# Performance work log

Hardware: AMD Instinct MI355X
Metric: run time of the kernel (lower is better)

The kernel has to match this reference:

```python
import jax, jax.numpy as jnp
import numpy as np

S, D, A, H, C = 2048, 256, 64, 8, 64  # seq_len, node_dim, num_aux, num_heads, num_channels
QUAT = 4
N_TYPES = 3  # nodes, aux, rot


def _linear_params(key, out_dim, in_dim, use_bias=True):
    kw, kb = jax.random.split(key)
    lim = 1.0 / np.sqrt(in_dim)
    W = jax.random.uniform(kw, (out_dim, in_dim), minval=-lim, maxval=lim, dtype=jnp.float32)
    if not use_bias:
        return W, None
    b = jax.random.uniform(kb, (out_dim,), minval=-lim, maxval=lim, dtype=jnp.float32)
    return W, b


def setup_inputs() -> dict:
    key = jax.random.key(0)
    ks = jax.random.split(key, 8)
    nodes = jax.random.normal(ks[0], (S, D), dtype=jnp.float32)
    aux = jax.random.normal(ks[1], (S, A), dtype=jnp.float32)
    rot = jax.random.normal(ks[2], (S, QUAT), dtype=jnp.float32)
    W_nodes, b_nodes = _linear_params(ks[3], H * C * 2, D)
    W_aux, b_aux = _linear_params(ks[4], H * C * 2, A)
    W_rot, _ = _linear_params(ks[5], H * C * 2, QUAT, use_bias=False)
    W_val, b_val = _linear_params(ks[6], D * H * N_TYPES, D)
    return {
        "nodes": nodes, "aux": aux, "rot": rot,
        "W_nodes": W_nodes, "b_nodes": b_nodes,
        "W_aux": W_aux, "b_aux": b_aux,
        "W_rot": W_rot,
        "W_val": W_val, "b_val": b_val,
    }


def reference(nodes, aux, rot, W_nodes, b_nodes, W_aux, b_aux, W_rot, W_val, b_val):
    seq_len = nodes.shape[0]
    # values: (S, 3H, D)
    val = (nodes @ W_val.T + b_val).reshape(seq_len, N_TYPES * H, -1)
    # per-source k/q: each (S, H, C)
    nodes_k, nodes_q = jnp.split((nodes @ W_nodes.T + b_nodes).reshape(seq_len, H, -1), 2, -1)
    aux_k, aux_q = jnp.split((aux @ W_aux.T + b_aux).reshape(seq_len, H, -1), 2, -1)
    rot_k, rot_q = jnp.split((rot @ W_rot.T).reshape(seq_len, H, -1), 2, -1)
    # concat along head axis -> (S, 3H, C)
    k = jnp.concatenate([nodes_k, aux_k, rot_k], axis=-2)
    q = jnp.concatenate([nodes_q, aux_q, rot_q], axis=-2)
    # (S, S, 3H) score tensor, scaled by 1/sqrt(num_heads) as in the original
    logits = jnp.einsum('ihc,jhc->ijh', k, q) / jnp.sqrt(jnp.asarray(H, nodes.dtype))
    att = jax.nn.softmax(logits, axis=-2)  # softmax over the j (key) axis
    out = jnp.einsum('ijh,jhd->id', att, val)  # (S, D)
    return out
```

## Files before the change

### kernel.cpp

```cpp
#include <hip/hip_runtime.h>

#define S_LEN 2048
#define NHEAD 24
#define CDIM 64
#define DDIM 256

typedef _Float16 f16x8 __attribute__((ext_vector_type(8)));
typedef float f32x4 __attribute__((ext_vector_type(4)));

__device__ __forceinline__ ushort f2h(float f) {
    _Float16 h = (_Float16)f;
    return __builtin_bit_cast(ushort, h);
}
__device__ __forceinline__ uint pkh(float a, float b) {
    auto v = __builtin_amdgcn_cvt_pkrtz(a, b);
    return __builtin_bit_cast(uint, v);
}
__device__ __forceinline__ uint pk2(float a, float b) {
    return (uint)f2h(a) | ((uint)f2h(b) << 16);
}

__device__ __forceinline__ int4 cvt8(const float* __restrict__ p) {
    float4 a = *(const float4*)p;
    float4 b = *(const float4*)(p + 4);
    f16x8 h;
    h[0] = (_Float16)a.x; h[1] = (_Float16)a.y;
    h[2] = (_Float16)a.z; h[3] = (_Float16)a.w;
    h[4] = (_Float16)b.x; h[5] = (_Float16)b.y;
    h[6] = (_Float16)b.z; h[7] = (_Float16)b.w;
    return __builtin_bit_cast(int4, h);
}

__global__ __launch_bounds__(256) void prep_kernel(
    const float* __restrict__ nodes, const float* __restrict__ W_val,
    float* __restrict__ out, ushort* __restrict__ nodes16, ushort* __restrict__ Wval16)
{
    int idx = blockIdx.x * 256 + threadIdx.x;
    if (idx < 131072) {
        ((float4*)out)[idx] = float4{0.f, 0.f, 0.f, 0.f};
    } else if (idx < 196608) {
        int i = idx - 131072;
        *(int4*)&nodes16[i * 8] = cvt8(&nodes[i * 8]);
    } else {
        int i = idx - 196608;
        *(int4*)&Wval16[i * 8] = cvt8(&W_val[i * 8]);
    }
}

__global__ __launch_bounds__(256) void proj_kernel(
    const float* __restrict__ nodes, const float* __restrict__ W_nodes,
    const float* __restrict__ b_nodes,
    const float* __restrict__ aux, const float* __restrict__ W_aux,
    const float* __restrict__ b_aux,
    const float* __restrict__ rot, const float* __restrict__ W_rot,
    const ushort* __restrict__ nodes16, const ushort* __restrict__ Wval16,
    const float* __restrict__ b_val,
    ushort* __restrict__ Kbuf, ushort* __restrict__ Qbuf, ushort* __restrict__ Vt)
{
    __shared__ ushort Asub[128 * 72];
    __shared__ ushort Wsub[128 * 72];
    const int blk = blockIdx.x;
    const int tid = threadIdx.x;
    const int wave = tid >> 6, lane = tid & 63;
    const int g = lane >> 4, c = lane & 15;

    if (blk < 768) {
        const int wm = wave & 1, wn = wave >> 1;
        const int m0 = (blk / 48) * 128, n0 = (blk % 48) * 128;
        const int K = 256;

        f32x4 acc[16];
#pragma unroll
        for (int t = 0; t < 16; t++) acc[t] = f32x4{0, 0, 0, 0};

        for (int k0 = 0; k0 < K; k0 += 64) {
            __syncthreads();
#pragma unroll
            for (int q = 0; q < 4; q++) {
                int i = tid + 256 * q;
                int row = i >> 3, kc = (i & 7) * 8;
                *(int4*)&Asub[row * 72 + kc] = *(const int4*)&nodes16[(m0 + row) * K + k0 + kc];
                *(int4*)&Wsub[row * 72 + kc] = *(const int4*)&Wval16[(n0 + row) * K + k0 + kc];
            }
            __syncthreads();

            f16x8 af0[4], af1[4];
#pragma unroll
            for (int mt = 0; mt < 4; mt++) {
                const ushort* Ar = &Asub[(wm * 64 + mt * 16 + c) * 72 + g * 8];
                af0[mt] = *(const f16x8*)Ar;
                af1[mt] = *(const f16x8*)(Ar + 32);
            }
#pragma unroll
            for (int nt = 0; nt < 4; nt++) {
                const ushort* Wr = &Wsub[(wn * 64 + nt * 16 + c) * 72 + g * 8];
                f16x8 bf0 = *(const f16x8*)Wr;
                f16x8 bf1 = *(const f16x8*)(Wr + 32);
#pragma unroll
                for (int mt = 0; mt < 4; mt++) {
                    acc[mt * 4 + nt] = __builtin_amdgcn_mfma_f32_16x16x32_f16(af0[mt], bf0, acc[mt * 4 + nt], 0, 0, 0);
                    acc[mt * 4 + nt] = __builtin_amdgcn_mfma_f32_16x16x32_f16(af1[mt], bf1, acc[mt * 4 + nt], 0, 0, 0);
                }
            }
        }

#pragma unroll
        for (int nt = 0; nt < 4; nt++) {
            int n = n0 + wn * 64 + nt * 16 + c;
            float bv = b_val[n];
            int h = n >> 8, d = n & 255;
#pragma unroll
            for (int mt = 0; mt < 4; mt++) {
                int m = m0 + wm * 64 + mt * 16 + g * 4;
                f32x4 v = acc[mt * 4 + nt];
                uint2 pw;
                pw.x = pk2(v[0] + bv, v[1] + bv);
                pw.y = pk2(v[2] + bv, v[3] + bv);
                *(uint2*)&Vt[(h * DDIM + d) * S_LEN + m] = pw;
            }
        }
    } else if (blk < 1792) {
        const int sub = blk - 768;
        const float *A, *W, *b;
        int K, hbase;
        if (sub < 512) { A = nodes; W = W_nodes; b = b_nodes; K = 256; hbase = 0; }
        else           { A = aux;   W = W_aux;   b = b_aux;   K = 64;  hbase = 8; }
        const int t5 = sub & 511;
        const int m0 = (t5 >> 4) * 64, n0 = (t5 & 15) * 64;
        const int srow = tid >> 2;
        const int skk = (tid & 3) * 8;

        f32x4 acc[4] = {f32x4{0,0,0,0}, f32x4{0,0,0,0}, f32x4{0,0,0,0}, f32x4{0,0,0,0}};

        for (int k0 = 0; k0 < K; k0 += 32) {
            __syncthreads();
            *(int4*)&Asub[srow * 40 + skk] = cvt8(&A[(m0 + srow) * K + k0 + skk]);
            *(int4*)&Wsub[srow * 40 + skk] = cvt8(&W[(n0 + srow) * K + k0 + skk]);
            __syncthreads();
            f16x8 af = *(const f16x8*)&Asub[(wave * 16 + c) * 40 + g * 8];
#pragma unroll
            for (int t = 0; t < 4; t++) {
                f16x8 bf = *(const f16x8*)&Wsub[(t * 16 + c) * 40 + g * 8];
                acc[t] = __builtin_amdgcn_mfma_f32_16x16x32_f16(af, bf, acc[t], 0, 0, 0);
            }
        }

#pragma unroll
        for (int t = 0; t < 4; t++) {
            int n = n0 + t * 16 + c;
            float bv = b[n];
#pragma unroll
            for (int r = 0; r < 4; r++) {
                int m = m0 + wave * 16 + g * 4 + r;
                ushort u = f2h(acc[t][r] + bv);
                int h = hbase + (n >> 7);
                int cc = n & 127;
                if (cc < 64) Kbuf[(h * S_LEN + m) * CDIM + cc] = u;
                else         Qbuf[(h * S_LEN + m) * CDIM + cc - 64] = u;
            }
        }
    } else {
        int u = (blk - 1792) * 256 + tid;
        int i = u >> 7;
        int n8 = (u & 127) * 8;
        float4 r = *(const float4*)&rot[i * 4];
        ushort pv[8];
#pragma unroll
        for (int q = 0; q < 8; q++) {
            float4 w = *(const float4*)&W_rot[(n8 + q) * 4];
            pv[q] = f2h(r.x * w.x + r.y * w.y + r.z * w.z + r.w * w.w);
        }
        int h = 16 + (n8 >> 7), cc = n8 & 127;
        int4 pkt = *(int4*)pv;
        if (cc < 64) *(int4*)&Kbuf[(h * S_LEN + i) * CDIM + cc] = pkt;
        else         *(int4*)&Qbuf[(h * S_LEN + i) * CDIM + cc - 64] = pkt;
    }
}

__global__ __launch_bounds__(256) void flash_kernel(
    const ushort* __restrict__ Kbuf, const ushort* __restrict__ Qbuf,
    const ushort* __restrict__ Vt, float* __restrict__ out)
{
    __shared__ ushort Qlds[2][64 * 72];
    __shared__ ushort Plds[2][64 * 72];
    __shared__ float  Alds[2][64];
    __shared__ int    Need[2][4] __attribute__((aligned(16)));

    const int tid = threadIdx.x;
    const int wave = tid >> 6, lane = tid & 63;
    const int g = lane >> 4, c = lane & 15;
    const int lin = blockIdx.y * 32 + blockIdx.x;
    const int xcd = lin & 7;
    const int slot = lin >> 3;
    const int h = xcd * 3 + (slot >> 5);
    const int i0 = (slot & 31) * 64;
    const float SC = 0.51006973f;
    const float THR = 8.0f;

    const ushort* Krow = &Kbuf[(h * S_LEN + i0 + wave * 16 + c) * CDIM + g * 8];
    f16x8 ka0 = *(const f16x8*)Krow;
    f16x8 ka1 = *(const f16x8*)(Krow + 32);

    const ushort* Vbase = &Vt[(h * DDIM + wave * 64 + c) * S_LEN + g * 8];

    const int qi0 = tid, qi1 = tid + 256;
    const int qr0 = qi0 >> 3, qc0 = (qi0 & 7) * 8;
    const int qr1 = qi1 >> 3, qc1 = (qi1 & 7) * 8;

    *(int4*)&Qlds[0][qr0 * 72 + qc0] =
        *(const int4*)&Qbuf[(h * S_LEN + qr0) * CDIM + qc0];
    *(int4*)&Qlds[0][qr1 * 72 + qc1] =
        *(const int4*)&Qbuf[(h * S_LEN + qr1) * CDIM + qc1];
    __syncthreads();

    f32x4 acc[16];
#pragma unroll
    for (int t = 0; t < 16; t++) acc[t] = f32x4{0, 0, 0, 0};
    float mrow = -1e30f, lrow = 0.f;

    for (int j0 = 0; j0 < S_LEN; j0 += 64) {
        const int cur = (j0 >> 6) & 1, nxt = cur ^ 1;

        const int jn = j0 + 64;
        int4 qn0 = *(const int4*)&Qbuf[(h * S_LEN + jn + qr0) * CDIM + qc0];
        int4 qn1 = *(const int4*)&Qbuf[(h * S_LEN + jn + qr1) * CDIM + qc1];

        f16x8 vf0[4], vf1[4];
#pragma unroll
        for (int t = 0; t < 4; t++) {
            const ushort* Vr = Vbase + (t * 16) * S_LEN + j0;
            vf0[t] = *(const f16x8*)Vr;
            vf1[t] = *(const f16x8*)(Vr + 32);
        }

        f32x4 Sf[4];
#pragma unroll
        for (int jc = 0; jc < 4; jc++) {
            const ushort* Qr = &Qlds[cur][(jc * 16 + c) * 72 + g * 8];
            f16x8 qb0 = *(const f16x8*)Qr;
            f16x8 qb1 = *(const f16x8*)(Qr + 32);
            f32x4 s = {0, 0, 0, 0};
            s = __builtin_amdgcn_mfma_f32_16x16x32_f16(qb0, ka0, s, 0, 0, 0);
            s = __builtin_amdgcn_mfma_f32_16x16x32_f16(qb1, ka1, s, 0, 0, 0);
            Sf[jc] = s * SC;
        }

        float tm = -1e30f;
#pragma unroll
        for (int jc = 0; jc < 4; jc++)
            tm = fmaxf(tm, fmaxf(fmaxf(Sf[jc][0], Sf[jc][1]),
                                 fmaxf(Sf[jc][2], Sf[jc][3])));
        tm = fmaxf(tm, __shfl_xor(tm, 16));
        tm = fmaxf(tm, __shfl_xor(tm, 32));

        const bool need = __any(tm > mrow + THR);
        float nm, alpha;
        if (need) {
            nm = fmaxf(tm, mrow);
            alpha = exp2f(mrow - nm);
        } else {
            nm = mrow;
            alpha = 1.0f;
        }
        if (lane == 0) Need[cur][wave] = need ? 1 : 0;

        float rs = 0.f;
#pragma unroll
        for (int jc = 0; jc < 4; jc++) {
            float p0 = exp2f(Sf[jc][0] - nm);
            float p1 = exp2f(Sf[jc][1] - nm);
            float p2 = exp2f(Sf[jc][2] - nm);
            float p3 = exp2f(Sf[jc][3] - nm);
            rs += (p0 + p1) + (p2 + p3);
            uint2 w;
            w.x = pkh(p0, p1);
            w.y = pkh(p2, p3);
            *(uint2*)&Plds[cur][(wave * 16 + c) * 72 + jc * 16 + g * 4] = w;
        }
        rs += __shfl_xor(rs, 16);
        rs += __shfl_xor(rs, 32);
        lrow = lrow * alpha + rs;
        mrow = nm;
        if (g == 0) Alds[cur][wave * 16 + c] = alpha;

        *(int4*)&Qlds[nxt][qr0 * 72 + qc0] = qn0;
        *(int4*)&Qlds[nxt][qr1 * 72 + qc1] = qn1;

        __syncthreads();

        int4 nf = *(const int4*)&Need[cur][0];
        if (nf.x | nf.y | nf.z | nf.w) {
#pragma unroll
            for (int b = 0; b < 4; b++) {
                f32x4 ab = *(const f32x4*)&Alds[cur][b * 16 + g * 4];
#pragma unroll
                for (int t = 0; t < 4; t++) acc[b * 4 + t] *= ab;
            }
        }

#pragma unroll
        for (int b = 0; b < 4; b++) {
            const ushort* Pr = &Plds[cur][(b * 16 + c) * 72 + g * 8];
            f16x8 pa0 = *(const f16x8*)Pr;
            f16x8 pa1 = *(const f16x8*)(Pr + 32);
#pragma unroll
            for (int t = 0; t < 4; t++) {
                acc[b * 4 + t] = __builtin_amdgcn_mfma_f32_16x16x32_f16(pa0, vf0[t], acc[b * 4 + t], 0, 0, 0);
                acc[b * 4 + t] = __builtin_amdgcn_mfma_f32_16x16x32_f16(pa1, vf1[t], acc[b * 4 + t], 0, 0, 0);
            }
        }
    }

    __syncthreads();
    if (g == 0) Alds[0][wave * 16 + c] = 1.0f / lrow;
    __syncthreads();
#pragma unroll
    for (int b = 0; b < 4; b++) {
        f32x4 lb = *(const f32x4*)&Alds[0][b * 16 + g * 4];
#pragma unroll
        for (int t = 0; t < 4; t++)
#pragma unroll
            for (int r = 0; r < 4; r++) {
                int i = i0 + b * 16 + g * 4 + r;
                int d = wave * 64 + t * 16 + c;
                atomicAdd(&out[i * DDIM + d], acc[b * 4 + t][r] * lb[r]);
            }
    }
}

extern "C" void kernel_launch(void* const* d_in, const int* in_sizes, int n_in,
                              void* d_out, int out_size, void* d_ws, size_t ws_size,
                              hipStream_t stream) {
    const float *nodes = 0, *aux = 0, *rot = 0, *W_nodes = 0, *b_nodes = 0,
                *W_aux = 0, *b_aux = 0, *W_rot = 0, *W_val = 0, *b_val = 0;
    int i1024[2] = {-1, -1};
    int n1024 = 0;
    for (int i = 0; i < n_in; ++i) {
        const float* p = (const float*)d_in[i];
        switch (in_sizes[i]) {
            case 524288:  nodes   = p; break;
            case 131072:  aux     = p; break;
            case 8192:    rot     = p; break;
            case 262144:  W_nodes = p; break;
            case 65536:   W_aux   = p; break;
            case 4096:    W_rot   = p; break;
            case 1572864: W_val   = p; break;
            case 6144:    b_val   = p; break;
            case 1024:    if (n1024 < 2) i1024[n1024] = i; n1024++; break;
            default: break;
        }
    }
    if (n1024 == 2) {
        b_nodes = (const float*)d_in[i1024[0]];
        b_aux   = (const float*)d_in[i1024[1]];
    }
    if (!nodes || !aux || !rot || !W_nodes || !b_nodes || !W_aux || !b_aux ||
        !W_rot || !W_val || !b_val) {
        nodes   = (const float*)d_in[0];
        aux     = (const float*)d_in[1];
        rot     = (const float*)d_in[2];
        W_nodes = (const float*)d_in[3];
        b_nodes = (const float*)d_in[4];
        W_aux   = (const float*)d_in[5];
        b_aux   = (const float*)d_in[6];
        W_rot   = (const float*)d_in[7];
        W_val   = (const float*)d_in[8];
        b_val   = (const float*)d_in[9];
    }
    float* out = (float*)d_out;

    float*  Opad = (float*)d_ws;
    ushort* Kbuf = (ushort*)(Opad + S_LEN * DDIM);
    ushort* Qbuf = Kbuf + NHEAD * S_LEN * CDIM;
    ushort* Vt   = Qbuf + NHEAD * S_LEN * CDIM;
    ushort* nodes16 = Vt + NHEAD * DDIM * S_LEN;
    ushort* Wval16  = nodes16 + 524288;

    dim3 blk(256);
    prep_kernel<<<dim3(1536), blk, 0, stream>>>(nodes, W_val, out, nodes16, Wval16);
    proj_kernel<<<dim3(2816), blk, 0, stream>>>(
        nodes, W_nodes, b_nodes, aux, W_aux, b_aux, rot, W_rot,
        nodes16, Wval16, b_val, Kbuf, Qbuf, Vt);
    flash_kernel<<<dim3(32, NHEAD), blk, 0, stream>>>(Kbuf, Qbuf, Vt, out);
}
```

Before: 252.7 us.

## Software-pipeline flash loop, fold score scale into K, defer row-sum reduce

The attention loop is restructured so each iteration computes the scores and softmax for the next tile while the PV MFMAs consume the previous tile's probabilities, with one barrier per iteration, a prologue and an epilogue. The 1/sqrt scale is folded into K during projection, which removes a multiply per score. The row-sum cross-lane shuffles are deferred until after the loop. Launch bounds now request 3 blocks per CU. Together these aim to overlap exp/softmax work with matrix work and cut per-iteration overhead, at the cost of higher register pressure and possible spills under the new occupancy constraint.

```diff
diff --git a/kernel.cpp b/kernel.cpp
--- a/kernel.cpp
+++ b/kernel.cpp
@@ -30,6 +30,8 @@
     h[6] = (_Float16)b.z; h[7] = (_Float16)b.w;
     return __builtin_bit_cast(int4, h);
 }
+
+#define SCALE_K 0.51006973f
 
 __global__ __launch_bounds__(256) void prep_kernel(
     const float* __restrict__ nodes, const float* __restrict__ W_val,
@@ -149,12 +151,13 @@
         for (int t = 0; t < 4; t++) {
             int n = n0 + t * 16 + c;
             float bv = b[n];
+            int h = hbase + (n >> 7);
+            int cc = n & 127;
+            float sc = (cc < 64) ? SCALE_K : 1.0f;
 #pragma unroll
             for (int r = 0; r < 4; r++) {
                 int m = m0 + wave * 16 + g * 4 + r;
-                ushort u = f2h(acc[t][r] + bv);
-                int h = hbase + (n >> 7);
-                int cc = n & 127;
+                ushort u = f2h((acc[t][r] + bv) * sc);
                 if (cc < 64) Kbuf[(h * S_LEN + m) * CDIM + cc] = u;
                 else         Qbuf[(h * S_LEN + m) * CDIM + cc - 64] = u;
             }
@@ -163,21 +166,23 @@
         int u = (blk - 1792) * 256 + tid;
         int i = u >> 7;
         int n8 = (u & 127) * 8;
+        int cc = n8 & 127;
+        float sc = (cc < 64) ? SCALE_K : 1.0f;
         float4 r = *(const float4*)&rot[i * 4];
         ushort pv[8];
 #pragma unroll
         for (int q = 0; q < 8; q++) {
             float4 w = *(const float4*)&W_rot[(n8 + q) * 4];
-            pv[q] = f2h(r.x * w.x + r.y * w.y + r.z * w.z + r.w * w.w);
-        }
-        int h = 16 + (n8 >> 7), cc = n8 & 127;
+            pv[q] = f2h((r.x * w.x + r.y * w.y + r.z * w.z + r.w * w.w) * sc);
+        }
+        int h = 16 + (n8 >> 7);
         int4 pkt = *(int4*)pv;
         if (cc < 64) *(int4*)&Kbuf[(h * S_LEN + i) * CDIM + cc] = pkt;
         else         *(int4*)&Qbuf[(h * S_LEN + i) * CDIM + cc - 64] = pkt;
     }
 }
 
-__global__ __launch_bounds__(256) void flash_kernel(
+__global__ __launch_bounds__(256, 3) void flash_kernel(
     const ushort* __restrict__ Kbuf, const ushort* __restrict__ Qbuf,
     const ushort* __restrict__ Vt, float* __restrict__ out)
 {
@@ -194,7 +199,6 @@
     const int slot = lin >> 3;
     const int h = xcd * 3 + (slot >> 5);
     const int i0 = (slot & 31) * 64;
-    const float SC = 0.51006973f;
     const float THR = 8.0f;
 
     const ushort* Krow = &Kbuf[(h * S_LEN + i0 + wave * 16 + c) * CDIM + g * 8];
@@ -202,49 +206,43 @@
     f16x8 ka1 = *(const f16x8*)(Krow + 32);
 
     const ushort* Vbase = &Vt[(h * DDIM + wave * 64 + c) * S_LEN + g * 8];
-
-    const int qi0 = tid, qi1 = tid + 256;
-    const int qr0 = qi0 >> 3, qc0 = (qi0 & 7) * 8;
-    const int qr1 = qi1 >> 3, qc1 = (qi1 & 7) * 8;
-
-    *(int4*)&Qlds[0][qr0 * 72 + qc0] =
-        *(const int4*)&Qbuf[(h * S_LEN + qr0) * CDIM + qc0];
-    *(int4*)&Qlds[0][qr1 * 72 + qc1] =
-        *(const int4*)&Qbuf[(h * S_LEN + qr1) * CDIM + qc1];
+    const ushort* Qh = &Qbuf[h * S_LEN * CDIM];
+
+    const int qr0 = tid >> 3, qc0 = (tid & 7) * 8;
+    const int qr1 = qr0 + 32;
+
+    *(int4*)&Qlds[0][qr0 * 72 + qc0] = *(const int4*)&Qh[qr0 * CDIM + qc0];
+    *(int4*)&Qlds[0][qr1 * 72 + qc0] = *(const int4*)&Qh[qr1 * CDIM + qc0];
+    int4 qn0 = *(const int4*)&Qh[(64 + qr0) * CDIM + qc0];
+    int4 qn1 = *(const int4*)&Qh[(64 + qr1) * CDIM + qc0];
+
+    f16x8 vf0[4], vf1[4];
+#pragma unroll
+    for (int u = 0; u < 4; u++) {
+        const ushort* Vr = Vbase + (u * 16) * S_LEN;
+        vf0[u] = *(const f16x8*)Vr;
+        vf1[u] = *(const f16x8*)(Vr + 32);
+    }
+
+    f32x4 acc[16];
+#pragma unroll
+    for (int u = 0; u < 16; u++) acc[u] = f32x4{0, 0, 0, 0};
+    float mrow = -1e30f, lrow = 0.f;
+
     __syncthreads();
 
-    f32x4 acc[16];
-#pragma unroll
-    for (int t = 0; t < 16; t++) acc[t] = f32x4{0, 0, 0, 0};
-    float mrow = -1e30f, lrow = 0.f;
-
-    for (int j0 = 0; j0 < S_LEN; j0 += 64) {
-        const int cur = (j0 >> 6) & 1, nxt = cur ^ 1;
-
-        const int jn = j0 + 64;
-        int4 qn0 = *(const int4*)&Qbuf[(h * S_LEN + jn + qr0) * CDIM + qc0];
-        int4 qn1 = *(const int4*)&Qbuf[(h * S_LEN + jn + qr1) * CDIM + qc1];
-
-        f16x8 vf0[4], vf1[4];
-#pragma unroll
-        for (int t = 0; t < 4; t++) {
-            const ushort* Vr = Vbase + (t * 16) * S_LEN + j0;
-            vf0[t] = *(const f16x8*)Vr;
-            vf1[t] = *(const f16x8*)(Vr + 32);
-        }
-
+    {
         f32x4 Sf[4];
 #pragma unroll
         for (int jc = 0; jc < 4; jc++) {
-            const ushort* Qr = &Qlds[cur][(jc * 16 + c) * 72 + g * 8];
+            const ushort* Qr = &Qlds[0][(jc * 16 + c) * 72 + g * 8];
             f16x8 qb0 = *(const f16x8*)Qr;
             f16x8 qb1 = *(const f16x8*)(Qr + 32);
             f32x4 s = {0, 0, 0, 0};
             s = __builtin_amdgcn_mfma_f32_16x16x32_f16(qb0, ka0, s, 0, 0, 0);
             s = __builtin_amdgcn_mfma_f32_16x16x32_f16(qb1, ka1, s, 0, 0, 0);
-            Sf[jc] = s * SC;
-        }
-
+            Sf[jc] = s;
+        }
         float tm = -1e30f;
 #pragma unroll
         for (int jc = 0; jc < 4; jc++)
@@ -252,18 +250,11 @@
                                  fmaxf(Sf[jc][2], Sf[jc][3])));
         tm = fmaxf(tm, __shfl_xor(tm, 16));
         tm = fmaxf(tm, __shfl_xor(tm, 32));
-
         const bool need = __any(tm > mrow + THR);
         float nm, alpha;
-        if (need) {
-            nm = fmaxf(tm, mrow);
-            alpha = exp2f(mrow - nm);
-        } else {
-            nm = mrow;
-            alpha = 1.0f;
-        }
-        if (lane == 0) Need[cur][wave] = need ? 1 : 0;
-
+        if (need) { nm = fmaxf(tm, mrow); alpha = exp2f(mrow - nm); }
+        else      { nm = mrow; alpha = 1.0f; }
+        if (lane == 0) Need[0][wave] = need ? 1 : 0;
         float rs = 0.f;
 #pragma unroll
         for (int jc = 0; jc < 4; jc++) {
@@ -275,18 +266,35 @@
             uint2 w;
             w.x = pkh(p0, p1);
             w.y = pkh(p2, p3);
-            *(uint2*)&Plds[cur][(wave * 16 + c) * 72 + jc * 16 + g * 4] = w;
-        }
-        rs += __shfl_xor(rs, 16);
-        rs += __shfl_xor(rs, 32);
+            *(uint2*)&Plds[0][(wave * 16 + c) * 72 + jc * 16 + g * 4] = w;
+        }
         lrow = lrow * alpha + rs;
         mrow = nm;
-        if (g == 0) Alds[cur][wave * 16 + c] = alpha;
-
-        *(int4*)&Qlds[nxt][qr0 * 72 + qc0] = qn0;
-        *(int4*)&Qlds[nxt][qr1 * 72 + qc1] = qn1;
-
+        if (g == 0) Alds[0][wave * 16 + c] = alpha;
+    }
+    *(int4*)&Qlds[1][qr0 * 72 + qc0] = qn0;
+    *(int4*)&Qlds[1][qr1 * 72 + qc0] = qn1;
+
+    for (int t = 0; t < 31; ++t) {
+        const int cur = t & 1, nxt = cur ^ 1;
         __syncthreads();
+
+        if (t < 30) {
+            qn0 = *(const int4*)&Qh[((t + 2) * 64 + qr0) * CDIM + qc0];
+            qn1 = *(const int4*)&Qh[((t + 2) * 64 + qr1) * CDIM + qc0];
+        }
+
+        f32x4 Sf[4];
+#pragma unroll
+        for (int jc = 0; jc < 4; jc++) {
+            const ushort* Qr = &Qlds[nxt][(jc * 16 + c) * 72 + g * 8];
+            f16x8 qb0 = *(const f16x8*)Qr;
+            f16x8 qb1 = *(const f16x8*)(Qr + 32);
+            f32x4 s = {0, 0, 0, 0};
+            s = __builtin_amdgcn_mfma_f32_16x16x32_f16(qb0, ka0, s, 0, 0, 0);
+            s = __builtin_amdgcn_mfma_f32_16x16x32_f16(qb1, ka1, s, 0, 0, 0);
+            Sf[jc] = s;
+        }
 
         int4 nf = *(const int4*)&Need[cur][0];
         if (nf.x | nf.y | nf.z | nf.w) {
@@ -294,7 +302,7 @@
             for (int b = 0; b < 4; b++) {
                 f32x4 ab = *(const f32x4*)&Alds[cur][b * 16 + g * 4];
 #pragma unroll
-                for (int t = 0; t < 4; t++) acc[b * 4 + t] *= ab;
+                for (int u = 0; u < 4; u++) acc[b * 4 + u] *= ab;
             }
         }
 
@@ -304,12 +312,82 @@
             f16x8 pa0 = *(const f16x8*)Pr;
             f16x8 pa1 = *(const f16x8*)(Pr + 32);
 #pragma unroll
-            for (int t = 0; t < 4; t++) {
-                acc[b * 4 + t] = __builtin_amdgcn_mfma_f32_16x16x32_f16(pa0, vf0[t], acc[b * 4 + t], 0, 0, 0);
-                acc[b * 4 + t] = __builtin_amdgcn_mfma_f32_16x16x32_f16(pa1, vf1[t], acc[b * 4 + t], 0, 0, 0);
-            }
-        }
-    }
+            for (int u = 0; u < 4; u++) {
+                acc[b * 4 + u] = __builtin_amdgcn_mfma_f32_16x16x32_f16(pa0, vf0[u], acc[b * 4 + u], 0, 0, 0);
+                acc[b * 4 + u] = __builtin_amdgcn_mfma_f32_16x16x32_f16(pa1, vf1[u], acc[b * 4 + u], 0, 0, 0);
+            }
+        }
+
+#pragma unroll
+        for (int u = 0; u < 4; u++) {
+            const ushort* Vr = Vbase + (u * 16) * S_LEN + (t + 1) * 64;
+            vf0[u] = *(const f16x8*)Vr;
+            vf1[u] = *(const f16x8*)(Vr + 32);
+        }
+
+        {
+            float tm = -1e30f;
+#pragma unroll
+            for (int jc = 0; jc < 4; jc++)
+                tm = fmaxf(tm, fmaxf(fmaxf(Sf[jc][0], Sf[jc][1]),
+                                     fmaxf(Sf[jc][2], Sf[jc][3])));
+            tm = fmaxf(tm, __shfl_xor(tm, 16));
+            tm = fmaxf(tm, __shfl_xor(tm, 32));
+            const bool need = __any(tm > mrow + THR);
+            float nm, alpha;
+            if (need) { nm = fmaxf(tm, mrow); alpha = exp2f(mrow - nm); }
+            else      { nm = mrow; alpha = 1.0f; }
+            if (lane == 0) Need[nxt][wave] = need ? 1 : 0;
+            float rs = 0.f;
+#pragma unroll
+            for (int jc = 0; jc < 4; jc++) {
+                float p0 = exp2f(Sf[jc][0] - nm);
+                float p1 = exp2f(Sf[jc][1] - nm);
+                float p2 = exp2f(Sf[jc][2] - nm);
+                float p3 = exp2f(Sf[jc][3] - nm);
+                rs += (p0 + p1) + (p2 + p3);
+                uint2 w;
+                w.x = pkh(p0, p1);
+                w.y = pkh(p2, p3);
+                *(uint2*)&Plds[nxt][(wave * 16 + c) * 72 + jc * 16 + g * 4] = w;
+            }
+            lrow = lrow * alpha + rs;
+            mrow = nm;
+            if (g == 0) Alds[nxt][wave * 16 + c] = alpha;
+        }
+
+        if (t < 30) {
+            *(int4*)&Qlds[cur][qr0 * 72 + qc0] = qn0;
+            *(int4*)&Qlds[cur][qr1 * 72 + qc0] = qn1;
+        }
+    }
+
+    __syncthreads();
+    {
+        int4 nf = *(const int4*)&Need[1][0];
+        if (nf.x | nf.y | nf.z | nf.w) {
+#pragma unroll
+            for (int b = 0; b < 4; b++) {
+                f32x4 ab = *(const f32x4*)&Alds[1][b * 16 + g * 4];
+#pragma unroll
+                for (int u = 0; u < 4; u++) acc[b * 4 + u] *= ab;
+            }
+        }
+#pragma unroll
+        for (int b = 0; b < 4; b++) {
+            const ushort* Pr = &Plds[1][(b * 16 + c) * 72 + g * 8];
+            f16x8 pa0 = *(const f16x8*)Pr;
+            f16x8 pa1 = *(const f16x8*)(Pr + 32);
+#pragma unroll
+            for (int u = 0; u < 4; u++) {
+                acc[b * 4 + u] = __builtin_amdgcn_mfma_f32_16x16x32_f16(pa0, vf0[u], acc[b * 4 + u], 0, 0, 0);
+                acc[b * 4 + u] = __builtin_amdgcn_mfma_f32_16x16x32_f16(pa1, vf1[u], acc[b * 4 + u], 0, 0, 0);
+            }
+        }
+    }
+
+    lrow += __shfl_xor(lrow, 16);
+    lrow += __shfl_xor(lrow, 32);
 
     __syncthreads();
     if (g == 0) Alds[0][wave * 16 + c] = 1.0f / lrow;
@@ -318,12 +396,12 @@
     for (int b = 0; b < 4; b++) {
         f32x4 lb = *(const f32x4*)&Alds[0][b * 16 + g * 4];
 #pragma unroll
-        for (int t = 0; t < 4; t++)
+        for (int u = 0; u < 4; u++)
 #pragma unroll
             for (int r = 0; r < 4; r++) {
                 int i = i0 + b * 16 + g * 4 + r;
-                int d = wave * 64 + t * 16 + c;
-                atomicAdd(&out[i * DDIM + d], acc[b * 4 + t][r] * lb[r]);
+                int d = wave * 64 + u * 16 + c;
+                atomicAdd(&out[i * DDIM + d], acc[b * 4 + u][r] * lb[r]);
             }
     }
 }
```

New measurement: 241.5 us. 1.05x faster.
